# Kernel optimization log

Hardware: AMD Instinct MI355X
Metric: run time of the kernel (lower is better)

## Reference

```python
import jax, jax.numpy as jnp
import numpy as np

N = 100_000          # nodes
E = 800_000          # edges
IN_DIM = 128
OUT_DIM = 128
H = 8                # heads
DK = OUT_DIM // H    # 16
T = 3                # node types
R = 8                # edge relation types
LN_EPS = 1e-5


def setup_inputs():
    key = jax.random.key(0)
    k = jax.random.split(key, 16)
    node_inp = jax.random.normal(k[0], (N, IN_DIM), dtype=jnp.float32)
    node_type = jax.random.randint(k[1], (N,), 0, T)
    edge_index = jax.random.randint(k[2], (2, E), 0, N)
    edge_type = jax.random.randint(k[3], (E,), 0, R)
    edge_sign = jax.random.randint(k[4], (E,), 0, 3) - 1      # values in {-1,0,1}
    edge_distance = jax.random.uniform(k[5], (E,), dtype=jnp.float32) * 2e5
    sc = 1.0 / np.sqrt(IN_DIM)
    Wq = jax.random.normal(k[6], (T, IN_DIM, OUT_DIM), dtype=jnp.float32) * sc
    Wk = jax.random.normal(k[7], (T, IN_DIM, OUT_DIM), dtype=jnp.float32) * sc
    Wv = jax.random.normal(k[8], (T, IN_DIM, OUT_DIM), dtype=jnp.float32) * sc
    bq = jnp.zeros((T, OUT_DIM), jnp.float32)
    bk = jnp.zeros((T, OUT_DIM), jnp.float32)
    bv = jnp.zeros((T, OUT_DIM), jnp.float32)
    rel_q = jax.random.normal(k[9], (R, H, DK), dtype=jnp.float32) * 0.2
    rel_k = jax.random.normal(k[10], (R, H, DK), dtype=jnp.float32) * 0.2
    rel_v = jax.random.normal(k[11], (R, H, DK), dtype=jnp.float32) * 0.2
    rel_bias = jnp.zeros((R, H), jnp.float32)
    ones = jnp.ones((H, DK), dtype=jnp.float32)
    sign_k_fixed = jnp.stack([-ones, ones], axis=0)   # [2,H,DK] buffers (neg,pos)
    sign_v_fixed = jnp.stack([-ones, ones], axis=0)
    sign_k_neutral = jnp.ones((H, DK), jnp.float32)
    sign_v_neutral = jnp.ones((H, DK), jnp.float32)
    dist_alpha = jnp.float32(0.1)
    dist_tau = jnp.float32(1e5)
    skip = jnp.ones((T,), jnp.float32)
    ln_gamma = jnp.ones((T, OUT_DIM), jnp.float32)
    ln_beta = jnp.zeros((T, OUT_DIM), jnp.float32)
    return dict(node_inp=node_inp, node_type=node_type, edge_index=edge_index,
                edge_type=edge_type, edge_sign=edge_sign, edge_distance=edge_distance,
                Wq=Wq, bq=bq, Wk=Wk, bk=bk, Wv=Wv, bv=bv,
                rel_q=rel_q, rel_k=rel_k, rel_v=rel_v, rel_bias=rel_bias,
                sign_k_fixed=sign_k_fixed, sign_v_fixed=sign_v_fixed,
                sign_k_neutral=sign_k_neutral, sign_v_neutral=sign_v_neutral,
                dist_alpha=dist_alpha, dist_tau=dist_tau, skip=skip,
                ln_gamma=ln_gamma, ln_beta=ln_beta)


def reference(node_inp, node_type, edge_index, edge_type, edge_sign, edge_distance,
              Wq, bq, Wk, bk, Wv, bv, rel_q, rel_k, rel_v, rel_bias,
              sign_k_fixed, sign_v_fixed, sign_k_neutral, sign_v_neutral,
              dist_alpha, dist_tau, skip, ln_gamma, ln_beta):
    src, dst = edge_index[0], edge_index[1]
    n = node_inp.shape[0]
    e = src.shape[0]
    # Per-node-type Q/K/V: compute projections for all types [N,T,O], select by type
    # (equivalent to the masked per-type Linear dispatch in the torch code).
    ar = jnp.arange(n)
    Q = (jnp.einsum('nd,tdo->nto', node_inp, Wq) + bq)[ar, node_type].reshape(n, H, DK)
    K = (jnp.einsum('nd,tdo->nto', node_inp, Wk) + bk)[ar, node_type].reshape(n, H, DK)
    V = (jnp.einsum('nd,tdo->nto', node_inp, Wv) + bv)[ar, node_type].reshape(n, H, DK)
    # sign dispatch: -1 -> 0 (neg), +1 -> 1 (pos), anything else -> 2 (neutral)
    sign_idx = jnp.where(edge_sign == -1, 0, jnp.where(edge_sign == 1, 1, 2))
    sign_k_all = jnp.concatenate([sign_k_fixed, sign_k_neutral[None]], axis=0)  # [3,H,DK]
    sign_v_all = jnp.concatenate([sign_v_fixed, sign_v_neutral[None]], axis=0)
    # edge-wise gather + relational modulation
    q_eff = Q[dst] * rel_q[edge_type]                               # [E,H,DK]
    k_eff = K[src] * rel_k[edge_type] * sign_k_all[sign_idx]
    v_eff = V[src] * rel_v[edge_type] * sign_v_all[sign_idx]
    scores = jnp.sum(q_eff * k_eff, axis=-1) / np.sqrt(DK)          # [E,H]
    scores = scores + rel_bias[edge_type]
    phi = dist_alpha * jnp.exp(-edge_distance / (dist_tau + 1e-9))
    scores = scores + phi[:, None]
    # segment softmax over destination nodes
    m = jax.ops.segment_max(scores, dst, num_segments=n)            # [N,H]
    m = jax.lax.stop_gradient(jnp.where(jnp.isfinite(m), m, 0.0))
    es = jnp.exp(scores - m[dst])
    Z = jax.ops.segment_sum(es, dst, num_segments=n)
    attn = es / (Z[dst] + 1e-9)
    # message scatter-aggregate
    msg = (v_eff * attn[:, :, None]).reshape(e, OUT_DIM)
    out = jax.ops.segment_sum(msg, dst, num_segments=n)             # [N,OUT_DIM]
    # per-type gated residual + per-type LayerNorm
    alpha = jax.nn.sigmoid(skip)[node_type][:, None]
    x = alpha * out + (1.0 - alpha) * node_inp
    mu = jnp.mean(x, axis=-1, keepdims=True)
    var = jnp.mean((x - mu) ** 2, axis=-1, keepdims=True)
    xn = (x - mu) * jax.lax.rsqrt(var + LN_EPS)
    return xn * ln_gamma[node_type] + ln_beta[node_type]
```

## Files before the change

kernel.cpp:

```cpp
#include <hip/hip_runtime.h>
#include <hip/hip_bf16.h>

typedef unsigned int uint;
typedef unsigned short ushort;
typedef unsigned long long ull;
typedef __attribute__((ext_vector_type(8))) short short8;
typedef __attribute__((ext_vector_type(4))) float f32x4;

#define WP_ELEMS 147456

__device__ __forceinline__ float bf2f(ushort u) { return __uint_as_float(((uint)u) << 16); }
__device__ __forceinline__ ushort f2bf(float f) {
  uint x = __float_as_uint(f);
  return (ushort)((x + 0x7fffu + ((x >> 16) & 1u)) >> 16);
}
__device__ __forceinline__ uint packbf(float a, float b) {
  return ((uint)f2bf(b) << 16) | (uint)f2bf(a);
}
__device__ __forceinline__ float bflo(uint u) { return __uint_as_float(u << 16); }
__device__ __forceinline__ float bfhi(uint u) { return __uint_as_float(u & 0xffff0000u); }

__global__ __launch_bounds__(256) void cvt_kernel(
    const float* __restrict__ wq, const float* __restrict__ wk, const float* __restrict__ wv,
    const float* __restrict__ rq, const float* __restrict__ rk, const float* __restrict__ rv,
    const float* __restrict__ skf, const float* __restrict__ svf,
    const float* __restrict__ skn, const float* __restrict__ svn,
    ushort* __restrict__ Wp, float* __restrict__ rkv) {
  int i = blockIdx.x * 256 + threadIdx.x;
  if (i < WP_ELEMS) {
    int j    = i & 7;
    int lane = (i >> 3) & 63;
    int ot   = (i >> 9) & 7;
    int ks   = (i >> 12) & 3;
    int mt   = i >> 14;
    int mat  = mt / 3;
    int t    = mt - mat * 3;
    int o = ot * 16 + (lane & 15);
    int d = ks * 32 + (lane >> 4) * 8 + j;
    const float* src = (mat == 0) ? wq : (mat == 1) ? wk : wv;
    Wp[i] = f2bf(src[t * 16384 + d * 128 + o]);
  }
  if (i < 3072) {
    int comb = i >> 7, c = i & 127;
    int et = comb / 3, sidx = comb - et * 3;
    float skv = (sidx < 2) ? skf[sidx * 128 + c] : skn[c];
    float svv = (sidx < 2) ? svf[sidx * 128 + c] : svn[c];
    float kkv = 0.25f * rq[et * 128 + c] * rk[et * 128 + c] * skv;
    float vvv = rv[et * 128 + c] * svv;
    int base = comb * 256 + (c >> 1) * 4 + (c & 1);
    rkv[base] = kkv;
    rkv[base + 2] = vvv;
  }
}

__global__ __launch_bounds__(256) void count_kernel(const int* __restrict__ ntype,
                                                    int* __restrict__ cnt, int N) {
  int i = blockIdx.x * 256 + threadIdx.x;
  int lane = threadIdx.x & 63;
  int t = (i < N) ? ntype[i] : -1;
#pragma unroll
  for (int tt = 0; tt < 3; ++tt) {
    ull mask = __ballot(t == tt);
    if (mask) {
      int leader = __ffsll((long long)mask) - 1;
      if (lane == leader) atomicAdd(&cnt[tt], __popcll(mask));
    }
  }
}

__global__ void offs_kernel(const int* __restrict__ cnt, int* __restrict__ off) {
  int o = 0;
  off[0] = 0;
  for (int t = 0; t < 3; ++t) {
    o += ((cnt[t] + 63) >> 6) << 6;
    off[t + 1] = o;
  }
}

__global__ __launch_bounds__(256) void fill_kernel(const int* __restrict__ ntype,
                                                   const int* __restrict__ off,
                                                   int* __restrict__ pos,
                                                   int* __restrict__ perm,
                                                   int* __restrict__ pinv, int N) {
  int i = blockIdx.x * 256 + threadIdx.x;
  int lane = threadIdx.x & 63;
  int t = (i < N) ? ntype[i] : -1;
#pragma unroll
  for (int tt = 0; tt < 3; ++tt) {
    ull mask = __ballot(t == tt);
    if (mask) {
      int leader = __ffsll((long long)mask) - 1;
      int base = 0;
      if (lane == leader) base = atomicAdd(&pos[tt], __popcll(mask));
      base = __shfl(base, leader);
      if (t == tt) {
        int rank = __popcll(mask & ((lane == 63) ? 0x7fffffffffffffffull
                                                 : ((1ull << lane) - 1ull)));
        int p = off[tt] + base + rank;
        perm[p] = i;
        pinv[i] = p;
      }
    }
  }
}

__global__ __launch_bounds__(256) void gemm_kernel(
    const float* __restrict__ X, const int* __restrict__ perm,
    const int* __restrict__ off, const ushort* __restrict__ Wp,
    const float* __restrict__ bq, const float* __restrict__ bk, const float* __restrict__ bv,
    float* __restrict__ Qp, uint* __restrict__ KVp) {
  __shared__ __align__(16) char smem[33792];
  __shared__ int prow[64];
  ushort* As = (ushort*)smem;
  float* tbuf = (float*)smem;
  const int tid = threadIdx.x;
  const int base = blockIdx.x * 64;
  const int off1 = off[1], off2 = off[2], off3 = off[3];
  if (base >= off3) return;
  const int t = (base >= off1) + (base >= off2);

  if (tid < 64) prow[tid] = perm[base + tid];
  __syncthreads();
#pragma unroll
  for (int pass = 0; pass < 8; ++pass) {
    int row = pass * 8 + (tid >> 5);
    int dw = tid & 31;
    int p = prow[row];
    uint ux = 0u, uy = 0u;
    if (p >= 0) {
      float4 xv = *(const float4*)(X + (size_t)p * 128 + dw * 4);
      ux = packbf(xv.x, xv.y);
      uy = packbf(xv.z, xv.w);
    }
    uint* s = (uint*)smem + row * 68 + dw * 2;
    s[0] = ux; s[1] = uy;
  }
  __syncthreads();

  const int lane = tid & 63;
  const int w = tid >> 6;
  const int m0 = w * 16;
  const int r = lane & 15;
  const int q = lane >> 4;

  short8 afrag[4];
#pragma unroll
  for (int ks = 0; ks < 4; ++ks)
    afrag[ks] = *(const short8*)(As + (m0 + r) * 136 + ks * 32 + q * 8);
  __syncthreads();

  float* tw = tbuf + w * 2112;
  uint4 ksave[4];
#pragma unroll
  for (int mat = 0; mat < 3; ++mat) {
    f32x4 acc[8];
#pragma unroll
    for (int ot = 0; ot < 8; ++ot) acc[ot] = (f32x4){0.f, 0.f, 0.f, 0.f};

    const ushort* wb = Wp + (size_t)(mat * 3 + t) * 16384 + lane * 8;
#pragma unroll
    for (int ks = 0; ks < 4; ++ks) {
      const ushort* wk_ = wb + ks * 4096;
#pragma unroll
      for (int ot = 0; ot < 8; ++ot) {
        short8 b = *(const short8*)(wk_ + ot * 512);
        acc[ot] = __builtin_amdgcn_mfma_f32_16x16x32_bf16(afrag[ks], b, acc[ot], 0, 0, 0);
      }
    }

    const float* bias = (mat == 0) ? bq : (mat == 1) ? bk : bv;
#pragma unroll
    for (int ot = 0; ot < 8; ++ot) {
      float bi = bias[t * 128 + ot * 16 + r];
#pragma unroll
      for (int reg = 0; reg < 4; ++reg)
        tw[(q * 4 + reg) * 132 + ot * 16 + r] = acc[ot][reg] + bi;
    }
    if (mat == 0) {
#pragma unroll
      for (int p = 0; p < 8; ++p) {
        int f = (p * 64 + lane) * 4;
        int row = f >> 7, col = f & 127;
        float4 val = *(const float4*)(tw + row * 132 + col);
        *(float4*)(Qp + (size_t)(base + m0 + row) * 128 + col) = val;
      }
    } else if (mat == 1) {
#pragma unroll
      for (int p = 0; p < 4; ++p) {
        int g = p * 64 + lane;
        int f = g * 8;
        int row = f >> 7, col = f & 127;
        const float* src = tw + row * 132 + col;
        float4 a4 = *(const float4*)(src);
        float4 b4 = *(const float4*)(src + 4);
        uint4 u;
        u.x = packbf(a4.x, a4.y);
        u.y = packbf(a4.z, a4.w);
        u.z = packbf(b4.x, b4.y);
        u.w = packbf(b4.z, b4.w);
        ksave[p] = u;
      }
    } else {
#pragma unroll
      for (int p = 0; p < 4; ++p) {
        int g = p * 64 + lane;
        int f = g * 8;
        int row = f >> 7, col = f & 127;
        const float* src = tw + row * 132 + col;
        float4 a4 = *(const float4*)(src);
        float4 b4 = *(const float4*)(src + 4);
        uint4 v4;
        v4.x = packbf(a4.x, a4.y);
        v4.y = packbf(a4.z, a4.w);
        v4.z = packbf(b4.x, b4.y);
        v4.w = packbf(b4.z, b4.w);
        uint4 w0, w1;
        w0.x = ksave[p].x; w0.y = v4.x; w0.z = ksave[p].y; w0.w = v4.y;
        w1.x = ksave[p].z; w1.y = v4.z; w1.z = ksave[p].w; w1.w = v4.w;
        uint* dstp = KVp + (size_t)(base + m0 + row) * 128 + col;
        *(uint4*)(dstp) = w0;
        *(uint4*)(dstp + 4) = w1;
      }
    }
  }
}

__global__ __launch_bounds__(256) void ecount_kernel(const int* __restrict__ edst,
                                                     int* __restrict__ ecnt, int E) {
  int e = blockIdx.x * 256 + threadIdx.x;
  if (e < E) atomicAdd(&ecnt[edst[e]], 1);
}

__global__ __launch_bounds__(256) void csum_kernel(const int* __restrict__ ecnt,
                                                   int* __restrict__ csum, int N) {
  __shared__ int s[4];
  int basei = blockIdx.x * 1024;
  int tid = threadIdx.x;
  int v = 0;
#pragma unroll
  for (int k = 0; k < 4; ++k) {
    int i = basei + k * 256 + tid;
    if (i < N) v += ecnt[i];
  }
#pragma unroll
  for (int m = 1; m < 64; m <<= 1) v += __shfl_xor(v, m);
  if ((tid & 63) == 0) s[tid >> 6] = v;
  __syncthreads();
  if (tid == 0) csum[blockIdx.x] = s[0] + s[1] + s[2] + s[3];
}

__global__ __launch_bounds__(1024) void cscan_kernel(const int* __restrict__ csum,
                                                     int* __restrict__ coff,
                                                     int* __restrict__ rowptrN,
                                                     int NC, int E) {
  __shared__ int sd[32];
  int tid = threadIdx.x, lane = tid & 63, w = tid >> 6;
  int v = (tid < NC) ? csum[tid] : 0;
  int x = v;
#pragma unroll
  for (int d = 1; d < 64; d <<= 1) {
    int t = __shfl_up(x, d);
    if (lane >= d) x += t;
  }
  if (lane == 63) sd[w] = x;
  __syncthreads();
  if (w == 0 && lane < 16) {
    int y = sd[lane];
#pragma unroll
    for (int d = 1; d < 16; d <<= 1) {
      int t = __shfl_up(y, d);
      if (lane >= d) y += t;
    }
    sd[16 + lane] = y;
  }
  __syncthreads();
  int excl = ((w > 0) ? sd[16 + w - 1] : 0) + (x - v);
  if (tid < NC) coff[tid] = excl;
  if (tid == 0) rowptrN[0] = E;
}

__global__ __launch_bounds__(1024) void rowptr_kernel(const int* __restrict__ ecnt,
                                                      const int* __restrict__ coff,
                                                      int* __restrict__ rowptr,
                                                      int* __restrict__ cursor, int N) {
  __shared__ int sd[32];
  int basei = blockIdx.x * 1024;
  int tid = threadIdx.x, lane = tid & 63, w = tid >> 6;
  int i = basei + tid;
  int v = (i < N) ? ecnt[i] : 0;
  int x = v;
#pragma unroll
  for (int d = 1; d < 64; d <<= 1) {
    int t = __shfl_up(x, d);
    if (lane >= d) x += t;
  }
  if (lane == 63) sd[w] = x;
  __syncthreads();
  if (w == 0 && lane < 16) {
    int y = sd[lane];
#pragma unroll
    for (int d = 1; d < 16; d <<= 1) {
      int t = __shfl_up(y, d);
      if (lane >= d) y += t;
    }
    sd[16 + lane] = y;
  }
  __syncthreads();
  int excl = coff[blockIdx.x] + ((w > 0) ? sd[16 + w - 1] : 0) + (x - v);
  if (i < N) { rowptr[i] = excl; cursor[i] = excl; }
}

__global__ __launch_bounds__(256) void scatter_kernel(
    const int* __restrict__ esrc, const int* __restrict__ edst,
    const int* __restrict__ etype, const int* __restrict__ esign,
    const float* __restrict__ edist,
    const float* __restrict__ p_alpha, const float* __restrict__ p_tau,
    const int* __restrict__ pinv, int* __restrict__ cursor,
    int* __restrict__ esrc_s, int* __restrict__ emeta_s, float* __restrict__ ephi_s, int E) {
  int e = blockIdx.x * 256 + threadIdx.x;
  if (e >= E) return;
  int dst = edst[e];
  int p = atomicAdd(&cursor[dst], 1);
  int et = etype[e], sg = esign[e];
  int sidx = (sg == -1) ? 0 : ((sg == 1) ? 1 : 2);
  float parg = fminf(fmaxf(-edist[e] / (p_tau[0] + 1e-9f), -80.f), 0.f);
  esrc_s[p] = pinv[esrc[e]];
  emeta_s[p] = (et << 8) | (et * 3 + sidx);
  ephi_s[p] = p_alpha[0] * __expf(parg);
}

struct Pass {
  uint4 kv0, kv1;
  float4 t0, t1, t2, t3;
  float bias;
  int valid;
};

__device__ __forceinline__ Pass prefetch_pass(
    int idx, int n, int srcv, int metav, float phiv,
    const uint* __restrict__ KVp, const float* __restrict__ rkv,
    const float* __restrict__ rb, int cl) {
  Pass P;
  P.valid = (idx < n);
  int pe = __shfl(srcv, idx);
  int meta = __shfl(metav, idx);
  float phi = __shfl(phiv, idx);
  if (!P.valid) { pe = 0; meta = 0; phi = 0.f; }
  int comb = meta & 255;
  int et = meta >> 8;
  const uint* kvb = KVp + (size_t)pe * 128 + cl * 8;
  P.kv0 = *(const uint4*)(kvb);
  P.kv1 = *(const uint4*)(kvb + 4);
  const float* tb = rkv + comb * 256 + cl * 16;
  P.t0 = *(const float4*)(tb);
  P.t1 = *(const float4*)(tb + 4);
  P.t2 = *(const float4*)(tb + 8);
  P.t3 = *(const float4*)(tb + 12);
  P.bias = rb[et * 8 + (cl >> 1)] + phi;
  return P;
}

__device__ __forceinline__ void compute_pass(
    const Pass& P, const float4& q0, const float4& q1, float& z,
    float& a0, float& a1, float& a2, float& a3,
    float& a4, float& a5, float& a6, float& a7) {
  float k0 = bflo(P.kv0.x), k1 = bfhi(P.kv0.x);
  float v0 = bflo(P.kv0.y), v1 = bfhi(P.kv0.y);
  float k2 = bflo(P.kv0.z), k3 = bfhi(P.kv0.z);
  float v2 = bflo(P.kv0.w), v3 = bfhi(P.kv0.w);
  float k4 = bflo(P.kv1.x), k5 = bfhi(P.kv1.x);
  float v4 = bflo(P.kv1.y), v5 = bfhi(P.kv1.y);
  float k6 = bflo(P.kv1.z), k7 = bfhi(P.kv1.z);
  float v6 = bflo(P.kv1.w), v7 = bfhi(P.kv1.w);

  float part = q0.x * (k0 * P.t0.x);
  part = fmaf(q0.y, k1 * P.t0.y, part);
  part = fmaf(q0.z, k2 * P.t1.x, part);
  part = fmaf(q0.w, k3 * P.t1.y, part);
  part = fmaf(q1.x, k4 * P.t2.x, part);
  part = fmaf(q1.y, k5 * P.t2.y, part);
  part = fmaf(q1.z, k6 * P.t3.x, part);
  part = fmaf(q1.w, k7 * P.t3.y, part);
  part += __shfl_xor(part, 1);
  float score = fminf(part + P.bias, 80.f);
  float es = __expf(score);
  es = P.valid ? es : 0.f;
  z += es;
  a0 = fmaf(es, v0 * P.t0.z, a0);
  a1 = fmaf(es, v1 * P.t0.w, a1);
  a2 = fmaf(es, v2 * P.t1.z, a2);
  a3 = fmaf(es, v3 * P.t1.w, a3);
  a4 = fmaf(es, v4 * P.t2.z, a4);
  a5 = fmaf(es, v5 * P.t2.w, a5);
  a6 = fmaf(es, v6 * P.t3.z, a6);
  a7 = fmaf(es, v7 * P.t3.w, a7);
}

__global__ __launch_bounds__(256) void agg_kernel(
    const float* __restrict__ Qp, const uint* __restrict__ KVp,
    const int* __restrict__ pinv, const int* __restrict__ rowptr,
    const int* __restrict__ esrc_s, const int* __restrict__ emeta_s,
    const float* __restrict__ ephi_s,
    const float* __restrict__ rb, const float* __restrict__ rkv,
    const float* __restrict__ X, const int* __restrict__ ntype,
    const float* __restrict__ skip, const float* __restrict__ gamma,
    const float* __restrict__ beta, float* __restrict__ y, int N) {
  int dst = blockIdx.x * 4 + (threadIdx.x >> 6);
  if (dst >= N) return;
  int lane = threadIdx.x & 63;
  int g = lane >> 4;
  int cl = lane & 15;
  int c0 = cl * 8;

  int pq = pinv[dst];
  const float* qb = Qp + (size_t)pq * 128 + c0;
  float4 q0 = *(const float4*)(qb);
  float4 q1 = *(const float4*)(qb + 4);

  float a0 = 0.f, a1 = 0.f, a2 = 0.f, a3 = 0.f;
  float a4 = 0.f, a5 = 0.f, a6 = 0.f, a7 = 0.f;
  float z = 0.f;

  int row0 = rowptr[dst], row1 = rowptr[dst + 1];
  for (int bb = row0; bb < row1; bb += 64) {
    int n = min(64, row1 - bb);
    int srcv = 0, metav = 0;
    float phiv = 0.f;
    if (lane < n) {
      srcv = esrc_s[bb + lane];
      metav = emeta_s[bb + lane];
      phiv = ephi_s[bb + lane];
    }
    int np = (n + 3) >> 2;
    Pass A = prefetch_pass(g, n, srcv, metav, phiv, KVp, rkv, rb, cl);
    int p = 0;
    while (true) {
      if (p + 1 < np) {
        Pass B = prefetch_pass((p + 1) * 4 + g, n, srcv, metav, phiv, KVp, rkv, rb, cl);
        compute_pass(A, q0, q1, z, a0, a1, a2, a3, a4, a5, a6, a7);
        A = B;
        ++p;
      } else {
        compute_pass(A, q0, q1, z, a0, a1, a2, a3, a4, a5, a6, a7);
        break;
      }
    }
  }

#pragma unroll
  for (int m = 16; m < 64; m <<= 1) {
    a0 += __shfl_xor(a0, m); a1 += __shfl_xor(a1, m);
    a2 += __shfl_xor(a2, m); a3 += __shfl_xor(a3, m);
    a4 += __shfl_xor(a4, m); a5 += __shfl_xor(a5, m);
    a6 += __shfl_xor(a6, m); a7 += __shfl_xor(a7, m);
    z  += __shfl_xor(z, m);
  }

  if (lane < 16) {
    float inv = 1.0f / (z + 1e-9f);
    float o0 = a0 * inv, o1 = a1 * inv, o2 = a2 * inv, o3 = a3 * inv;
    float o4 = a4 * inv, o5 = a5 * inv, o6 = a6 * inv, o7 = a7 * inv;

    int t = ntype[dst];
    float a = 1.0f / (1.0f + __expf(-skip[t]));
    float b = 1.0f - a;
    const float* xb = X + (size_t)dst * 128 + c0;
    float4 x0 = *(const float4*)(xb);
    float4 x1 = *(const float4*)(xb + 4);
    float w0 = a * o0 + b * x0.x, w1 = a * o1 + b * x0.y;
    float w2 = a * o2 + b * x0.z, w3 = a * o3 + b * x0.w;
    float w4 = a * o4 + b * x1.x, w5 = a * o5 + b * x1.y;
    float w6 = a * o6 + b * x1.z, w7 = a * o7 + b * x1.w;

    float sum = w0 + w1 + w2 + w3 + w4 + w5 + w6 + w7;
    float sq = w0 * w0 + w1 * w1 + w2 * w2 + w3 * w3 +
               w4 * w4 + w5 * w5 + w6 * w6 + w7 * w7;
#pragma unroll
    for (int m = 1; m < 16; m <<= 1) {
      sum += __shfl_xor(sum, m);
      sq  += __shfl_xor(sq, m);
    }
    float mean = sum * (1.0f / 128.0f);
    float var = fmaxf(sq * (1.0f / 128.0f) - mean * mean, 0.0f);
    float rstd = rsqrtf(var + 1e-5f);

    const float* gb = gamma + t * 128 + c0;
    const float* bb2 = beta + t * 128 + c0;
    float4 g0 = *(const float4*)(gb);
    float4 g1 = *(const float4*)(gb + 4);
    float4 be0 = *(const float4*)(bb2);
    float4 be1 = *(const float4*)(bb2 + 4);
    float4 r0, r1;
    r0.x = (w0 - mean) * rstd * g0.x + be0.x;
    r0.y = (w1 - mean) * rstd * g0.y + be0.y;
    r0.z = (w2 - mean) * rstd * g0.z + be0.z;
    r0.w = (w3 - mean) * rstd * g0.w + be0.w;
    r1.x = (w4 - mean) * rstd * g1.x + be1.x;
    r1.y = (w5 - mean) * rstd * g1.y + be1.y;
    r1.z = (w6 - mean) * rstd * g1.z + be1.z;
    r1.w = (w7 - mean) * rstd * g1.w + be1.w;
    float* yb = y + (size_t)dst * 128 + c0;
    *(float4*)(yb) = r0;
    *(float4*)(yb + 4) = r1;
  }
}

extern "C" void kernel_launch(void* const* d_in, const int* in_sizes, int n_in,
                              void* d_out, int out_size, void* d_ws, size_t ws_size,
                              hipStream_t stream) {
  const float* X     = (const float*)d_in[0];
  const int*   ntype = (const int*)d_in[1];
  const int*   eidx  = (const int*)d_in[2];
  const int*   etype = (const int*)d_in[3];
  const int*   esign = (const int*)d_in[4];
  const float* edist = (const float*)d_in[5];
  const float* wq = (const float*)d_in[6];
  const float* bq = (const float*)d_in[7];
  const float* wk = (const float*)d_in[8];
  const float* bk = (const float*)d_in[9];
  const float* wv = (const float*)d_in[10];
  const float* bv = (const float*)d_in[11];
  const float* rq = (const float*)d_in[12];
  const float* rk = (const float*)d_in[13];
  const float* rv = (const float*)d_in[14];
  const float* rb = (const float*)d_in[15];

  const int N = in_sizes[1];
  const int E = in_sizes[3];
  const int NP = N + 192;
  const int NC = (N + 1023) / 1024;

  float* ws = (float*)d_ws;
  float* Qp   = ws;
  uint*  KVp  = (uint*)(Qp + (size_t)NP * 128);
  float* rkv  = (float*)(KVp + (size_t)NP * 128);
  ushort* Wp  = (ushort*)(rkv + 6144);
  int* cnt    = (int*)(Wp + WP_ELEMS);
  int* pos    = cnt + 4;
  int* ecnt   = pos + 4;
  int* perm   = ecnt + N;
  int* pinv   = perm + NP;
  int* off    = pinv + N;
  int* rowptr = off + 4;
  int* cursor = rowptr + N + 1;
  int* csum   = cursor + N;
  int* coff   = csum + 1024;
  int* esrc_s = coff + 1024;
  int* emeta_s = esrc_s + E;
  float* ephi_s = (float*)(emeta_s + E);

  hipMemsetAsync(cnt, 0, (size_t)(8 + N) * sizeof(int), stream);
  hipMemsetAsync(perm, 0xFF, (size_t)NP * sizeof(int), stream);

  cvt_kernel<<<(WP_ELEMS + 255) / 256, 256, 0, stream>>>(
      wq, wk, wv, rq, rk, rv, (const float*)d_in[16], (const float*)d_in[17],
      (const float*)d_in[18], (const float*)d_in[19], Wp, rkv);
  count_kernel<<<(N + 255) / 256, 256, 0, stream>>>(ntype, cnt, N);
  offs_kernel<<<1, 1, 0, stream>>>(cnt, off);
  fill_kernel<<<(N + 255) / 256, 256, 0, stream>>>(ntype, off, pos, perm, pinv, N);

  ecount_kernel<<<(E + 255) / 256, 256, 0, stream>>>(eidx + E, ecnt, E);
  csum_kernel<<<NC, 256, 0, stream>>>(ecnt, csum, N);
  cscan_kernel<<<1, 1024, 0, stream>>>(csum, coff, rowptr + N, NC, E);
  rowptr_kernel<<<NC, 1024, 0, stream>>>(ecnt, coff, rowptr, cursor, N);
  scatter_kernel<<<(E + 255) / 256, 256, 0, stream>>>(
      eidx, eidx + E, etype, esign, edist, (const float*)d_in[20], (const float*)d_in[21],
      pinv, cursor, esrc_s, emeta_s, ephi_s, E);

  gemm_kernel<<<(N + 255) / 64, 256, 0, stream>>>(X, perm, off, Wp, bq, bk, bv, Qp, KVp);

  agg_kernel<<<(N + 3) / 4, 256, 0, stream>>>(Qp, KVp, pinv, rowptr, esrc_s, emeta_s,
                                              ephi_s, rb, rkv, X, ntype,
                                              (const float*)d_in[22], (const float*)d_in[23],
                                              (const float*)d_in[24], (float*)d_out, N);
}
```

Before: 585.8 us.

## Batch edge gathers four-deep, pack edge metadata, use persistent aggregation waves

The aggregation loop now issues up to four K/V row gathers before consuming any of them, replacing the one-ahead prefetch, to raise memory-level parallelism on random source-node reads. Edge source index, relation combo and edge type are packed into one int, dropping one 4-byte stream per edge from the scatter and aggregation kernels. The aggregation kernel becomes a grid-stride persistent kernel with 2048 blocks and a launch-bounds occupancy hint of 6. The deeper batching raises register pressure, and the packed index assumes fewer than 2^18 nodes.

```diff
diff --git a/kernel.cpp b/kernel.cpp
--- a/kernel.cpp
+++ b/kernel.cpp
@@ -9,7 +9,6 @@
 
 #define WP_ELEMS 147456
 
-__device__ __forceinline__ float bf2f(ushort u) { return __uint_as_float(((uint)u) << 16); }
 __device__ __forceinline__ ushort f2bf(float f) {
   uint x = __float_as_uint(f);
   return (ushort)((x + 0x7fffu + ((x >> 16) & 1u)) >> 16);
@@ -316,7 +315,7 @@
     const float* __restrict__ edist,
     const float* __restrict__ p_alpha, const float* __restrict__ p_tau,
     const int* __restrict__ pinv, int* __restrict__ cursor,
-    int* __restrict__ esrc_s, int* __restrict__ emeta_s, float* __restrict__ ephi_s, int E) {
+    int* __restrict__ epk_s, float* __restrict__ ephi_s, int E) {
   int e = blockIdx.x * 256 + threadIdx.x;
   if (e >= E) return;
   int dst = edst[e];
@@ -324,184 +323,187 @@
   int et = etype[e], sg = esign[e];
   int sidx = (sg == -1) ? 0 : ((sg == 1) ? 1 : 2);
   float parg = fminf(fmaxf(-edist[e] / (p_tau[0] + 1e-9f), -80.f), 0.f);
-  esrc_s[p] = pinv[esrc[e]];
-  emeta_s[p] = (et << 8) | (et * 3 + sidx);
+  epk_s[p] = pinv[esrc[e]] | ((et * 3 + sidx) << 18) | (et << 23);
   ephi_s[p] = p_alpha[0] * __expf(parg);
 }
 
-struct Pass {
-  uint4 kv0, kv1;
-  float4 t0, t1, t2, t3;
-  float bias;
-  int valid;
-};
-
-__device__ __forceinline__ Pass prefetch_pass(
-    int idx, int n, int srcv, int metav, float phiv,
+template <int B>
+__device__ __forceinline__ void agg_batch(
+    int p0, int g, int cl, int n, int srcv, float phiv,
     const uint* __restrict__ KVp, const float* __restrict__ rkv,
-    const float* __restrict__ rb, int cl) {
-  Pass P;
-  P.valid = (idx < n);
-  int pe = __shfl(srcv, idx);
-  int meta = __shfl(metav, idx);
-  float phi = __shfl(phiv, idx);
-  if (!P.valid) { pe = 0; meta = 0; phi = 0.f; }
-  int comb = meta & 255;
-  int et = meta >> 8;
-  const uint* kvb = KVp + (size_t)pe * 128 + cl * 8;
-  P.kv0 = *(const uint4*)(kvb);
-  P.kv1 = *(const uint4*)(kvb + 4);
-  const float* tb = rkv + comb * 256 + cl * 16;
-  P.t0 = *(const float4*)(tb);
-  P.t1 = *(const float4*)(tb + 4);
-  P.t2 = *(const float4*)(tb + 8);
-  P.t3 = *(const float4*)(tb + 12);
-  P.bias = rb[et * 8 + (cl >> 1)] + phi;
-  return P;
-}
-
-__device__ __forceinline__ void compute_pass(
-    const Pass& P, const float4& q0, const float4& q1, float& z,
+    const float* __restrict__ rb,
+    const float4& q0, const float4& q1, float& z,
     float& a0, float& a1, float& a2, float& a3,
     float& a4, float& a5, float& a6, float& a7) {
-  float k0 = bflo(P.kv0.x), k1 = bfhi(P.kv0.x);
-  float v0 = bflo(P.kv0.y), v1 = bfhi(P.kv0.y);
-  float k2 = bflo(P.kv0.z), k3 = bfhi(P.kv0.z);
-  float v2 = bflo(P.kv0.w), v3 = bfhi(P.kv0.w);
-  float k4 = bflo(P.kv1.x), k5 = bfhi(P.kv1.x);
-  float v4 = bflo(P.kv1.y), v5 = bfhi(P.kv1.y);
-  float k6 = bflo(P.kv1.z), k7 = bfhi(P.kv1.z);
-  float v6 = bflo(P.kv1.w), v7 = bfhi(P.kv1.w);
-
-  float part = q0.x * (k0 * P.t0.x);
-  part = fmaf(q0.y, k1 * P.t0.y, part);
-  part = fmaf(q0.z, k2 * P.t1.x, part);
-  part = fmaf(q0.w, k3 * P.t1.y, part);
-  part = fmaf(q1.x, k4 * P.t2.x, part);
-  part = fmaf(q1.y, k5 * P.t2.y, part);
-  part = fmaf(q1.z, k6 * P.t3.x, part);
-  part = fmaf(q1.w, k7 * P.t3.y, part);
-  part += __shfl_xor(part, 1);
-  float score = fminf(part + P.bias, 80.f);
-  float es = __expf(score);
-  es = P.valid ? es : 0.f;
-  z += es;
-  a0 = fmaf(es, v0 * P.t0.z, a0);
-  a1 = fmaf(es, v1 * P.t0.w, a1);
-  a2 = fmaf(es, v2 * P.t1.z, a2);
-  a3 = fmaf(es, v3 * P.t1.w, a3);
-  a4 = fmaf(es, v4 * P.t2.z, a4);
-  a5 = fmaf(es, v5 * P.t2.w, a5);
-  a6 = fmaf(es, v6 * P.t3.z, a6);
-  a7 = fmaf(es, v7 * P.t3.w, a7);
-}
-
-__global__ __launch_bounds__(256) void agg_kernel(
+  const int i0 = p0 * 4 + g;
+  int pk[B];
+  float ph[B];
+#pragma unroll
+  for (int k = 0; k < B; ++k) {
+    pk[k] = __shfl(srcv, i0 + 4 * k);
+    ph[k] = __shfl(phiv, i0 + 4 * k);
+  }
+  uint4 ka[B], kb[B];
+#pragma unroll
+  for (int k = 0; k < B; ++k) {
+    const uint* bp = KVp + (size_t)(pk[k] & 0x3ffff) * 128 + cl * 8;
+    ka[k] = *(const uint4*)(bp);
+    kb[k] = *(const uint4*)(bp + 4);
+  }
+#pragma unroll
+  for (int k = 0; k < B; ++k) {
+    int comb = (pk[k] >> 18) & 31;
+    int et = (pk[k] >> 23) & 7;
+    const float* tb = rkv + comb * 256 + cl * 16;
+    float4 t0 = *(const float4*)(tb);
+    float4 t1 = *(const float4*)(tb + 4);
+    float4 t2 = *(const float4*)(tb + 8);
+    float4 t3 = *(const float4*)(tb + 12);
+    float bias = rb[et * 8 + (cl >> 1)] + ph[k];
+    float k0 = bflo(ka[k].x), k1 = bfhi(ka[k].x);
+    float v0 = bflo(ka[k].y), v1 = bfhi(ka[k].y);
+    float k2 = bflo(ka[k].z), k3 = bfhi(ka[k].z);
+    float v2 = bflo(ka[k].w), v3 = bfhi(ka[k].w);
+    float k4 = bflo(kb[k].x), k5 = bfhi(kb[k].x);
+    float v4 = bflo(kb[k].y), v5 = bfhi(kb[k].y);
+    float k6 = bflo(kb[k].z), k7 = bfhi(kb[k].z);
+    float v6 = bflo(kb[k].w), v7 = bfhi(kb[k].w);
+    float part = q0.x * (k0 * t0.x);
+    part = fmaf(q0.y, k1 * t0.y, part);
+    part = fmaf(q0.z, k2 * t1.x, part);
+    part = fmaf(q0.w, k3 * t1.y, part);
+    part = fmaf(q1.x, k4 * t2.x, part);
+    part = fmaf(q1.y, k5 * t2.y, part);
+    part = fmaf(q1.z, k6 * t3.x, part);
+    part = fmaf(q1.w, k7 * t3.y, part);
+    part += __shfl_xor(part, 1);
+    float score = fminf(part + bias, 80.f);
+    float es = ((i0 + 4 * k) < n) ? __expf(score) : 0.f;
+    z += es;
+    a0 = fmaf(es, v0 * t0.z, a0);
+    a1 = fmaf(es, v1 * t0.w, a1);
+    a2 = fmaf(es, v2 * t1.z, a2);
+    a3 = fmaf(es, v3 * t1.w, a3);
+    a4 = fmaf(es, v4 * t2.z, a4);
+    a5 = fmaf(es, v5 * t2.w, a5);
+    a6 = fmaf(es, v6 * t3.z, a6);
+    a7 = fmaf(es, v7 * t3.w, a7);
+  }
+}
+
+__global__ __launch_bounds__(256, 6) void agg_kernel(
     const float* __restrict__ Qp, const uint* __restrict__ KVp,
     const int* __restrict__ pinv, const int* __restrict__ rowptr,
-    const int* __restrict__ esrc_s, const int* __restrict__ emeta_s,
-    const float* __restrict__ ephi_s,
+    const int* __restrict__ epk_s, const float* __restrict__ ephi_s,
     const float* __restrict__ rb, const float* __restrict__ rkv,
     const float* __restrict__ X, const int* __restrict__ ntype,
     const float* __restrict__ skip, const float* __restrict__ gamma,
-    const float* __restrict__ beta, float* __restrict__ y, int N) {
-  int dst = blockIdx.x * 4 + (threadIdx.x >> 6);
-  if (dst >= N) return;
-  int lane = threadIdx.x & 63;
-  int g = lane >> 4;
-  int cl = lane & 15;
-  int c0 = cl * 8;
-
-  int pq = pinv[dst];
-  const float* qb = Qp + (size_t)pq * 128 + c0;
-  float4 q0 = *(const float4*)(qb);
-  float4 q1 = *(const float4*)(qb + 4);
-
-  float a0 = 0.f, a1 = 0.f, a2 = 0.f, a3 = 0.f;
-  float a4 = 0.f, a5 = 0.f, a6 = 0.f, a7 = 0.f;
-  float z = 0.f;
-
-  int row0 = rowptr[dst], row1 = rowptr[dst + 1];
-  for (int bb = row0; bb < row1; bb += 64) {
-    int n = min(64, row1 - bb);
-    int srcv = 0, metav = 0;
-    float phiv = 0.f;
-    if (lane < n) {
-      srcv = esrc_s[bb + lane];
-      metav = emeta_s[bb + lane];
-      phiv = ephi_s[bb + lane];
-    }
-    int np = (n + 3) >> 2;
-    Pass A = prefetch_pass(g, n, srcv, metav, phiv, KVp, rkv, rb, cl);
-    int p = 0;
-    while (true) {
-      if (p + 1 < np) {
-        Pass B = prefetch_pass((p + 1) * 4 + g, n, srcv, metav, phiv, KVp, rkv, rb, cl);
-        compute_pass(A, q0, q1, z, a0, a1, a2, a3, a4, a5, a6, a7);
-        A = B;
-        ++p;
-      } else {
-        compute_pass(A, q0, q1, z, a0, a1, a2, a3, a4, a5, a6, a7);
-        break;
-      }
-    }
-  }
-
-#pragma unroll
-  for (int m = 16; m < 64; m <<= 1) {
-    a0 += __shfl_xor(a0, m); a1 += __shfl_xor(a1, m);
-    a2 += __shfl_xor(a2, m); a3 += __shfl_xor(a3, m);
-    a4 += __shfl_xor(a4, m); a5 += __shfl_xor(a5, m);
-    a6 += __shfl_xor(a6, m); a7 += __shfl_xor(a7, m);
-    z  += __shfl_xor(z, m);
-  }
-
-  if (lane < 16) {
-    float inv = 1.0f / (z + 1e-9f);
-    float o0 = a0 * inv, o1 = a1 * inv, o2 = a2 * inv, o3 = a3 * inv;
-    float o4 = a4 * inv, o5 = a5 * inv, o6 = a6 * inv, o7 = a7 * inv;
-
-    int t = ntype[dst];
-    float a = 1.0f / (1.0f + __expf(-skip[t]));
-    float b = 1.0f - a;
-    const float* xb = X + (size_t)dst * 128 + c0;
-    float4 x0 = *(const float4*)(xb);
-    float4 x1 = *(const float4*)(xb + 4);
-    float w0 = a * o0 + b * x0.x, w1 = a * o1 + b * x0.y;
-    float w2 = a * o2 + b * x0.z, w3 = a * o3 + b * x0.w;
-    float w4 = a * o4 + b * x1.x, w5 = a * o5 + b * x1.y;
-    float w6 = a * o6 + b * x1.z, w7 = a * o7 + b * x1.w;
-
-    float sum = w0 + w1 + w2 + w3 + w4 + w5 + w6 + w7;
-    float sq = w0 * w0 + w1 * w1 + w2 * w2 + w3 * w3 +
-               w4 * w4 + w5 * w5 + w6 * w6 + w7 * w7;
-#pragma unroll
-    for (int m = 1; m < 16; m <<= 1) {
-      sum += __shfl_xor(sum, m);
-      sq  += __shfl_xor(sq, m);
-    }
-    float mean = sum * (1.0f / 128.0f);
-    float var = fmaxf(sq * (1.0f / 128.0f) - mean * mean, 0.0f);
-    float rstd = rsqrtf(var + 1e-5f);
-
-    const float* gb = gamma + t * 128 + c0;
-    const float* bb2 = beta + t * 128 + c0;
-    float4 g0 = *(const float4*)(gb);
-    float4 g1 = *(const float4*)(gb + 4);
-    float4 be0 = *(const float4*)(bb2);
-    float4 be1 = *(const float4*)(bb2 + 4);
-    float4 r0, r1;
-    r0.x = (w0 - mean) * rstd * g0.x + be0.x;
-    r0.y = (w1 - mean) * rstd * g0.y + be0.y;
-    r0.z = (w2 - mean) * rstd * g0.z + be0.z;
-    r0.w = (w3 - mean) * rstd * g0.w + be0.w;
-    r1.x = (w4 - mean) * rstd * g1.x + be1.x;
-    r1.y = (w5 - mean) * rstd * g1.y + be1.y;
-    r1.z = (w6 - mean) * rstd * g1.z + be1.z;
-    r1.w = (w7 - mean) * rstd * g1.w + be1.w;
-    float* yb = y + (size_t)dst * 128 + c0;
-    *(float4*)(yb) = r0;
-    *(float4*)(yb + 4) = r1;
+    const float* __restrict__ beta, float* __restrict__ y, int N, int nwaves) {
+  const int wid = blockIdx.x * 4 + (threadIdx.x >> 6);
+  const int lane = threadIdx.x & 63;
+  const int g = lane >> 4;
+  const int cl = lane & 15;
+  const int c0 = cl * 8;
+
+  for (int dst = wid; dst < N; dst += nwaves) {
+    int pq = pinv[dst];
+    const float* qb = Qp + (size_t)pq * 128 + c0;
+    float4 q0 = *(const float4*)(qb);
+    float4 q1 = *(const float4*)(qb + 4);
+
+    float a0 = 0.f, a1 = 0.f, a2 = 0.f, a3 = 0.f;
+    float a4 = 0.f, a5 = 0.f, a6 = 0.f, a7 = 0.f;
+    float z = 0.f;
+
+    int row0 = rowptr[dst], row1 = rowptr[dst + 1];
+    for (int bb = row0; bb < row1; bb += 64) {
+      int n = min(64, row1 - bb);
+      int srcv = 0;
+      float phiv = 0.f;
+      if (lane < n) {
+        srcv = epk_s[bb + lane];
+        phiv = ephi_s[bb + lane];
+      }
+      int np = (n + 3) >> 2;
+      int p0 = 0;
+      while (p0 < np) {
+        int rem = np - p0;
+        if (rem >= 4) {
+          agg_batch<4>(p0, g, cl, n, srcv, phiv, KVp, rkv, rb, q0, q1, z,
+                       a0, a1, a2, a3, a4, a5, a6, a7);
+          p0 += 4;
+        } else if (rem == 3) {
+          agg_batch<3>(p0, g, cl, n, srcv, phiv, KVp, rkv, rb, q0, q1, z,
+                       a0, a1, a2, a3, a4, a5, a6, a7);
+          p0 += 3;
+        } else if (rem == 2) {
+          agg_batch<2>(p0, g, cl, n, srcv, phiv, KVp, rkv, rb, q0, q1, z,
+                       a0, a1, a2, a3, a4, a5, a6, a7);
+          p0 += 2;
+        } else {
+          agg_batch<1>(p0, g, cl, n, srcv, phiv, KVp, rkv, rb, q0, q1, z,
+                       a0, a1, a2, a3, a4, a5, a6, a7);
+          p0 += 1;
+        }
+      }
+    }
+
+#pragma unroll
+    for (int m = 16; m < 64; m <<= 1) {
+      a0 += __shfl_xor(a0, m); a1 += __shfl_xor(a1, m);
+      a2 += __shfl_xor(a2, m); a3 += __shfl_xor(a3, m);
+      a4 += __shfl_xor(a4, m); a5 += __shfl_xor(a5, m);
+      a6 += __shfl_xor(a6, m); a7 += __shfl_xor(a7, m);
+      z  += __shfl_xor(z, m);
+    }
+
+    if (lane < 16) {
+      float inv = 1.0f / (z + 1e-9f);
+      float o0 = a0 * inv, o1 = a1 * inv, o2 = a2 * inv, o3 = a3 * inv;
+      float o4 = a4 * inv, o5 = a5 * inv, o6 = a6 * inv, o7 = a7 * inv;
+
+      int t = ntype[dst];
+      float a = 1.0f / (1.0f + __expf(-skip[t]));
+      float b = 1.0f - a;
+      const float* xb = X + (size_t)dst * 128 + c0;
+      float4 x0 = *(const float4*)(xb);
+      float4 x1 = *(const float4*)(xb + 4);
+      float w0 = a * o0 + b * x0.x, w1 = a * o1 + b * x0.y;
+      float w2 = a * o2 + b * x0.z, w3 = a * o3 + b * x0.w;
+      float w4 = a * o4 + b * x1.x, w5 = a * o5 + b * x1.y;
+      float w6 = a * o6 + b * x1.z, w7 = a * o7 + b * x1.w;
+
+      float sum = w0 + w1 + w2 + w3 + w4 + w5 + w6 + w7;
+      float sq = w0 * w0 + w1 * w1 + w2 * w2 + w3 * w3 +
+                 w4 * w4 + w5 * w5 + w6 * w6 + w7 * w7;
+#pragma unroll
+      for (int m = 1; m < 16; m <<= 1) {
+        sum += __shfl_xor(sum, m);
+        sq  += __shfl_xor(sq, m);
+      }
+      float mean = sum * (1.0f / 128.0f);
+      float var = fmaxf(sq * (1.0f / 128.0f) - mean * mean, 0.0f);
+      float rstd = rsqrtf(var + 1e-5f);
+
+      const float* gb = gamma + t * 128 + c0;
+      const float* bb2 = beta + t * 128 + c0;
+      float4 g0 = *(const float4*)(gb);
+      float4 g1 = *(const float4*)(gb + 4);
+      float4 be0 = *(const float4*)(bb2);
+      float4 be1 = *(const float4*)(bb2 + 4);
+      float4 r0, r1;
+      r0.x = (w0 - mean) * rstd * g0.x + be0.x;
+      r0.y = (w1 - mean) * rstd * g0.y + be0.y;
+      r0.z = (w2 - mean) * rstd * g0.z + be0.z;
+      r0.w = (w3 - mean) * rstd * g0.w + be0.w;
+      r1.x = (w4 - mean) * rstd * g1.x + be1.x;
+      r1.y = (w5 - mean) * rstd * g1.y + be1.y;
+      r1.z = (w6 - mean) * rstd * g1.z + be1.z;
+      r1.w = (w7 - mean) * rstd * g1.w + be1.w;
+      float* yb = y + (size_t)dst * 128 + c0;
+      *(float4*)(yb) = r0;
+      *(float4*)(yb + 4) = r1;
+    }
   }
 }
 
@@ -545,9 +547,8 @@
   int* cursor = rowptr + N + 1;
   int* csum   = cursor + N;
   int* coff   = csum + 1024;
-  int* esrc_s = coff + 1024;
-  int* emeta_s = esrc_s + E;
-  float* ephi_s = (float*)(emeta_s + E);
+  int* epk_s  = coff + 1024;
+  float* ephi_s = (float*)(epk_s + E);
 
   hipMemsetAsync(cnt, 0, (size_t)(8 + N) * sizeof(int), stream);
   hipMemsetAsync(perm, 0xFF, (size_t)NP * sizeof(int), stream);
@@ -565,12 +566,14 @@
   rowptr_kernel<<<NC, 1024, 0, stream>>>(ecnt, coff, rowptr, cursor, N);
   scatter_kernel<<<(E + 255) / 256, 256, 0, stream>>>(
       eidx, eidx + E, etype, esign, edist, (const float*)d_in[20], (const float*)d_in[21],
-      pinv, cursor, esrc_s, emeta_s, ephi_s, E);
+      pinv, cursor, epk_s, ephi_s, E);
 
   gemm_kernel<<<(N + 255) / 64, 256, 0, stream>>>(X, perm, off, Wp, bq, bk, bv, Qp, KVp);
 
-  agg_kernel<<<(N + 3) / 4, 256, 0, stream>>>(Qp, KVp, pinv, rowptr, esrc_s, emeta_s,
-                                              ephi_s, rb, rkv, X, ntype,
-                                              (const float*)d_in[22], (const float*)d_in[23],
-                                              (const float*)d_in[24], (float*)d_out, N);
-}
+  const int nblocks = 2048;
+  agg_kernel<<<nblocks, 256, 0, stream>>>(Qp, KVp, pinv, rowptr, epk_s, ephi_s,
+                                          rb, rkv, X, ntype,
+                                          (const float*)d_in[22], (const float*)d_in[23],
+                                          (const float*)d_in[24], (float*)d_out, N,
+                                          nblocks * 4);
+}
```

New measurement: 836.5 us. +42.8%, slower.

## Pack edge src and metadata into one word; persistent grid-stride aggregation

Applied to the files above, without the earlier changes.

Source index, combined relation/sign index and edge type are packed into a single 32-bit word per sorted edge. This removes one array write in the scatter step and one load per edge in aggregation. The aggregation kernel becomes persistent: a fixed grid of 2048 blocks walks destination nodes with a grid stride instead of launching one wave per node. The bit packing assumes node indices fit in 18 bits and that a fixed grid balances the per-node degree variation well.

```diff
diff --git a/kernel.cpp b/kernel.cpp
--- a/kernel.cpp
+++ b/kernel.cpp
@@ -9,7 +9,6 @@
 
 #define WP_ELEMS 147456
 
-__device__ __forceinline__ float bf2f(ushort u) { return __uint_as_float(((uint)u) << 16); }
 __device__ __forceinline__ ushort f2bf(float f) {
   uint x = __float_as_uint(f);
   return (ushort)((x + 0x7fffu + ((x >> 16) & 1u)) >> 16);
@@ -316,7 +315,7 @@
     const float* __restrict__ edist,
     const float* __restrict__ p_alpha, const float* __restrict__ p_tau,
     const int* __restrict__ pinv, int* __restrict__ cursor,
-    int* __restrict__ esrc_s, int* __restrict__ emeta_s, float* __restrict__ ephi_s, int E) {
+    int* __restrict__ epk_s, float* __restrict__ ephi_s, int E) {
   int e = blockIdx.x * 256 + threadIdx.x;
   if (e >= E) return;
   int dst = edst[e];
@@ -324,8 +323,7 @@
   int et = etype[e], sg = esign[e];
   int sidx = (sg == -1) ? 0 : ((sg == 1) ? 1 : 2);
   float parg = fminf(fmaxf(-edist[e] / (p_tau[0] + 1e-9f), -80.f), 0.f);
-  esrc_s[p] = pinv[esrc[e]];
-  emeta_s[p] = (et << 8) | (et * 3 + sidx);
+  epk_s[p] = pinv[esrc[e]] | ((et * 3 + sidx) << 18) | (et << 23);
   ephi_s[p] = p_alpha[0] * __expf(parg);
 }
 
@@ -337,17 +335,17 @@
 };
 
 __device__ __forceinline__ Pass prefetch_pass(
-    int idx, int n, int srcv, int metav, float phiv,
+    int idx, int n, int pkv, float phiv,
     const uint* __restrict__ KVp, const float* __restrict__ rkv,
     const float* __restrict__ rb, int cl) {
   Pass P;
   P.valid = (idx < n);
-  int pe = __shfl(srcv, idx);
-  int meta = __shfl(metav, idx);
+  int pk = __shfl(pkv, idx);
   float phi = __shfl(phiv, idx);
-  if (!P.valid) { pe = 0; meta = 0; phi = 0.f; }
-  int comb = meta & 255;
-  int et = meta >> 8;
+  if (!P.valid) { pk = 0; phi = 0.f; }
+  int pe = pk & 0x3ffff;
+  int comb = (pk >> 18) & 31;
+  int et = (pk >> 23) & 7;
   const uint* kvb = KVp + (size_t)pe * 128 + cl * 8;
   P.kv0 = *(const uint4*)(kvb);
   P.kv1 = *(const uint4*)(kvb + 4);
@@ -399,109 +397,108 @@
 __global__ __launch_bounds__(256) void agg_kernel(
     const float* __restrict__ Qp, const uint* __restrict__ KVp,
     const int* __restrict__ pinv, const int* __restrict__ rowptr,
-    const int* __restrict__ esrc_s, const int* __restrict__ emeta_s,
-    const float* __restrict__ ephi_s,
+    const int* __restrict__ epk_s, const float* __restrict__ ephi_s,
     const float* __restrict__ rb, const float* __restrict__ rkv,
     const float* __restrict__ X, const int* __restrict__ ntype,
     const float* __restrict__ skip, const float* __restrict__ gamma,
-    const float* __restrict__ beta, float* __restrict__ y, int N) {
-  int dst = blockIdx.x * 4 + (threadIdx.x >> 6);
-  if (dst >= N) return;
-  int lane = threadIdx.x & 63;
-  int g = lane >> 4;
-  int cl = lane & 15;
-  int c0 = cl * 8;
-
-  int pq = pinv[dst];
-  const float* qb = Qp + (size_t)pq * 128 + c0;
-  float4 q0 = *(const float4*)(qb);
-  float4 q1 = *(const float4*)(qb + 4);
-
-  float a0 = 0.f, a1 = 0.f, a2 = 0.f, a3 = 0.f;
-  float a4 = 0.f, a5 = 0.f, a6 = 0.f, a7 = 0.f;
-  float z = 0.f;
-
-  int row0 = rowptr[dst], row1 = rowptr[dst + 1];
-  for (int bb = row0; bb < row1; bb += 64) {
-    int n = min(64, row1 - bb);
-    int srcv = 0, metav = 0;
-    float phiv = 0.f;
-    if (lane < n) {
-      srcv = esrc_s[bb + lane];
-      metav = emeta_s[bb + lane];
-      phiv = ephi_s[bb + lane];
-    }
-    int np = (n + 3) >> 2;
-    Pass A = prefetch_pass(g, n, srcv, metav, phiv, KVp, rkv, rb, cl);
-    int p = 0;
-    while (true) {
-      if (p + 1 < np) {
-        Pass B = prefetch_pass((p + 1) * 4 + g, n, srcv, metav, phiv, KVp, rkv, rb, cl);
-        compute_pass(A, q0, q1, z, a0, a1, a2, a3, a4, a5, a6, a7);
-        A = B;
-        ++p;
-      } else {
-        compute_pass(A, q0, q1, z, a0, a1, a2, a3, a4, a5, a6, a7);
-        break;
-      }
-    }
-  }
-
-#pragma unroll
-  for (int m = 16; m < 64; m <<= 1) {
-    a0 += __shfl_xor(a0, m); a1 += __shfl_xor(a1, m);
-    a2 += __shfl_xor(a2, m); a3 += __shfl_xor(a3, m);
-    a4 += __shfl_xor(a4, m); a5 += __shfl_xor(a5, m);
-    a6 += __shfl_xor(a6, m); a7 += __shfl_xor(a7, m);
-    z  += __shfl_xor(z, m);
-  }
-
-  if (lane < 16) {
-    float inv = 1.0f / (z + 1e-9f);
-    float o0 = a0 * inv, o1 = a1 * inv, o2 = a2 * inv, o3 = a3 * inv;
-    float o4 = a4 * inv, o5 = a5 * inv, o6 = a6 * inv, o7 = a7 * inv;
-
-    int t = ntype[dst];
-    float a = 1.0f / (1.0f + __expf(-skip[t]));
-    float b = 1.0f - a;
-    const float* xb = X + (size_t)dst * 128 + c0;
-    float4 x0 = *(const float4*)(xb);
-    float4 x1 = *(const float4*)(xb + 4);
-    float w0 = a * o0 + b * x0.x, w1 = a * o1 + b * x0.y;
-    float w2 = a * o2 + b * x0.z, w3 = a * o3 + b * x0.w;
-    float w4 = a * o4 + b * x1.x, w5 = a * o5 + b * x1.y;
-    float w6 = a * o6 + b * x1.z, w7 = a * o7 + b * x1.w;
-
-    float sum = w0 + w1 + w2 + w3 + w4 + w5 + w6 + w7;
-    float sq = w0 * w0 + w1 * w1 + w2 * w2 + w3 * w3 +
-               w4 * w4 + w5 * w5 + w6 * w6 + w7 * w7;
-#pragma unroll
-    for (int m = 1; m < 16; m <<= 1) {
-      sum += __shfl_xor(sum, m);
-      sq  += __shfl_xor(sq, m);
-    }
-    float mean = sum * (1.0f / 128.0f);
-    float var = fmaxf(sq * (1.0f / 128.0f) - mean * mean, 0.0f);
-    float rstd = rsqrtf(var + 1e-5f);
-
-    const float* gb = gamma + t * 128 + c0;
-    const float* bb2 = beta + t * 128 + c0;
-    float4 g0 = *(const float4*)(gb);
-    float4 g1 = *(const float4*)(gb + 4);
-    float4 be0 = *(const float4*)(bb2);
-    float4 be1 = *(const float4*)(bb2 + 4);
-    float4 r0, r1;
-    r0.x = (w0 - mean) * rstd * g0.x + be0.x;
-    r0.y = (w1 - mean) * rstd * g0.y + be0.y;
-    r0.z = (w2 - mean) * rstd * g0.z + be0.z;
-    r0.w = (w3 - mean) * rstd * g0.w + be0.w;
-    r1.x = (w4 - mean) * rstd * g1.x + be1.x;
-    r1.y = (w5 - mean) * rstd * g1.y + be1.y;
-    r1.z = (w6 - mean) * rstd * g1.z + be1.z;
-    r1.w = (w7 - mean) * rstd * g1.w + be1.w;
-    float* yb = y + (size_t)dst * 128 + c0;
-    *(float4*)(yb) = r0;
-    *(float4*)(yb + 4) = r1;
+    const float* __restrict__ beta, float* __restrict__ y, int N, int nwaves) {
+  const int wid = blockIdx.x * 4 + (threadIdx.x >> 6);
+  const int lane = threadIdx.x & 63;
+  const int g = lane >> 4;
+  const int cl = lane & 15;
+  const int c0 = cl * 8;
+
+  for (int dst = wid; dst < N; dst += nwaves) {
+    int pq = pinv[dst];
+    const float* qb = Qp + (size_t)pq * 128 + c0;
+    float4 q0 = *(const float4*)(qb);
+    float4 q1 = *(const float4*)(qb + 4);
+
+    float a0 = 0.f, a1 = 0.f, a2 = 0.f, a3 = 0.f;
+    float a4 = 0.f, a5 = 0.f, a6 = 0.f, a7 = 0.f;
+    float z = 0.f;
+
+    int row0 = rowptr[dst], row1 = rowptr[dst + 1];
+    for (int bb = row0; bb < row1; bb += 64) {
+      int n = min(64, row1 - bb);
+      int pkv = 0;
+      float phiv = 0.f;
+      if (lane < n) {
+        pkv = epk_s[bb + lane];
+        phiv = ephi_s[bb + lane];
+      }
+      int np = (n + 3) >> 2;
+      Pass A = prefetch_pass(g, n, pkv, phiv, KVp, rkv, rb, cl);
+      int p = 0;
+      while (true) {
+        if (p + 1 < np) {
+          Pass B = prefetch_pass((p + 1) * 4 + g, n, pkv, phiv, KVp, rkv, rb, cl);
+          compute_pass(A, q0, q1, z, a0, a1, a2, a3, a4, a5, a6, a7);
+          A = B;
+          ++p;
+        } else {
+          compute_pass(A, q0, q1, z, a0, a1, a2, a3, a4, a5, a6, a7);
+          break;
+        }
+      }
+    }
+
+#pragma unroll
+    for (int m = 16; m < 64; m <<= 1) {
+      a0 += __shfl_xor(a0, m); a1 += __shfl_xor(a1, m);
+      a2 += __shfl_xor(a2, m); a3 += __shfl_xor(a3, m);
+      a4 += __shfl_xor(a4, m); a5 += __shfl_xor(a5, m);
+      a6 += __shfl_xor(a6, m); a7 += __shfl_xor(a7, m);
+      z  += __shfl_xor(z, m);
+    }
+
+    if (lane < 16) {
+      float inv = 1.0f / (z + 1e-9f);
+      float o0 = a0 * inv, o1 = a1 * inv, o2 = a2 * inv, o3 = a3 * inv;
+      float o4 = a4 * inv, o5 = a5 * inv, o6 = a6 * inv, o7 = a7 * inv;
+
+      int t = ntype[dst];
+      float a = 1.0f / (1.0f + __expf(-skip[t]));
+      float b = 1.0f - a;
+      const float* xb = X + (size_t)dst * 128 + c0;
+      float4 x0 = *(const float4*)(xb);
+      float4 x1 = *(const float4*)(xb + 4);
+      float w0 = a * o0 + b * x0.x, w1 = a * o1 + b * x0.y;
+      float w2 = a * o2 + b * x0.z, w3 = a * o3 + b * x0.w;
+      float w4 = a * o4 + b * x1.x, w5 = a * o5 + b * x1.y;
+      float w6 = a * o6 + b * x1.z, w7 = a * o7 + b * x1.w;
+
+      float sum = w0 + w1 + w2 + w3 + w4 + w5 + w6 + w7;
+      float sq = w0 * w0 + w1 * w1 + w2 * w2 + w3 * w3 +
+                 w4 * w4 + w5 * w5 + w6 * w6 + w7 * w7;
+#pragma unroll
+      for (int m = 1; m < 16; m <<= 1) {
+        sum += __shfl_xor(sum, m);
+        sq  += __shfl_xor(sq, m);
+      }
+      float mean = sum * (1.0f / 128.0f);
+      float var = fmaxf(sq * (1.0f / 128.0f) - mean * mean, 0.0f);
+      float rstd = rsqrtf(var + 1e-5f);
+
+      const float* gb = gamma + t * 128 + c0;
+      const float* bb2 = beta + t * 128 + c0;
+      float4 g0 = *(const float4*)(gb);
+      float4 g1 = *(const float4*)(gb + 4);
+      float4 be0 = *(const float4*)(bb2);
+      float4 be1 = *(const float4*)(bb2 + 4);
+      float4 r0, r1;
+      r0.x = (w0 - mean) * rstd * g0.x + be0.x;
+      r0.y = (w1 - mean) * rstd * g0.y + be0.y;
+      r0.z = (w2 - mean) * rstd * g0.z + be0.z;
+      r0.w = (w3 - mean) * rstd * g0.w + be0.w;
+      r1.x = (w4 - mean) * rstd * g1.x + be1.x;
+      r1.y = (w5 - mean) * rstd * g1.y + be1.y;
+      r1.z = (w6 - mean) * rstd * g1.z + be1.z;
+      r1.w = (w7 - mean) * rstd * g1.w + be1.w;
+      float* yb = y + (size_t)dst * 128 + c0;
+      *(float4*)(yb) = r0;
+      *(float4*)(yb + 4) = r1;
+    }
   }
 }
 
@@ -545,9 +542,8 @@
   int* cursor = rowptr + N + 1;
   int* csum   = cursor + N;
   int* coff   = csum + 1024;
-  int* esrc_s = coff + 1024;
-  int* emeta_s = esrc_s + E;
-  float* ephi_s = (float*)(emeta_s + E);
+  int* epk_s  = coff + 1024;
+  float* ephi_s = (float*)(epk_s + E);
 
   hipMemsetAsync(cnt, 0, (size_t)(8 + N) * sizeof(int), stream);
   hipMemsetAsync(perm, 0xFF, (size_t)NP * sizeof(int), stream);
@@ -565,12 +561,14 @@
   rowptr_kernel<<<NC, 1024, 0, stream>>>(ecnt, coff, rowptr, cursor, N);
   scatter_kernel<<<(E + 255) / 256, 256, 0, stream>>>(
       eidx, eidx + E, etype, esign, edist, (const float*)d_in[20], (const float*)d_in[21],
-      pinv, cursor, esrc_s, emeta_s, ephi_s, E);
+      pinv, cursor, epk_s, ephi_s, E);
 
   gemm_kernel<<<(N + 255) / 64, 256, 0, stream>>>(X, perm, off, Wp, bq, bk, bv, Qp, KVp);
 
-  agg_kernel<<<(N + 3) / 4, 256, 0, stream>>>(Qp, KVp, pinv, rowptr, esrc_s, emeta_s,
-                                              ephi_s, rb, rkv, X, ntype,
-                                              (const float*)d_in[22], (const float*)d_in[23],
-                                              (const float*)d_in[24], (float*)d_out, N);
-}
+  const int nblocks = 2048;
+  agg_kernel<<<nblocks, 256, 0, stream>>>(Qp, KVp, pinv, rowptr, epk_s, ephi_s,
+                                          rb, rkv, X, ntype,
+                                          (const float*)d_in[22], (const float*)d_in[23],
+                                          (const float*)d_in[24], (float*)d_out, N,
+                                          nblocks * 4);
+}
```

Result: faster. 569.9 us (-2.7%).
